# Kernel optimization log

Hardware: AMD Instinct MI355X
Metric: run time of the kernel (lower is better)

The kernel has to match this reference:

```python
import jax, jax.numpy as jnp
import numpy as np

B, S, T, N, D, L = 8192, 10, 3, 65536, 128, 2  # batch, neigh len, node types, table size, embed_d, layers
NEG_SLOPE = 0.01  # torch LeakyReLU default


def setup_inputs() -> dict:
    key = jax.random.key(0)
    ks = jax.random.split(key, 6)
    return {
        "emb": jax.random.normal(ks[0], (T, N, D), jnp.float32) * 0.02,
        "Wih": jax.random.normal(ks[1], (L, T, D, D), jnp.float32) / np.sqrt(D).astype(np.float32),
        "Whh": jax.random.normal(ks[2], (L, T, D, D), jnp.float32) / np.sqrt(D).astype(np.float32),
        "bih": jnp.full((L, T, D), 0.1, jnp.float32),
        "bhh": jnp.full((L, T, D), 0.1, jnp.float32),
        "w_att": jax.random.normal(ks[3], (L, 2 * D), jnp.float32) / np.sqrt(2 * D).astype(np.float32),
        "ids": jax.random.randint(ks[4], (B,), 0, N),
        "neigh_idx": jax.random.randint(ks[5], (T, B, S), 0, N),
    }


def _rnn_mean(x, Wih_l, Whh_l, bih_l, bhh_l):
    """x: [T,B,S,D] neighbor embeds. torch nn.RNN(tanh): h_s = tanh(x_s@Wih^T + bih + h@Whh^T + bhh).
    Returns mean of all hidden states over time: [T,B,D]."""
    xs = jnp.moveaxis(x, 2, 0)  # [S, T, B, D]
    h0 = jnp.zeros((T, B, D), x.dtype)

    def step(h, x_s):
        h = jnp.tanh(jnp.einsum('tbd,ted->tbe', x_s, Wih_l) + bih_l[:, None, :]
                     + jnp.einsum('tbd,ted->tbe', h, Whh_l) + bhh_l[:, None, :])
        return h, h

    _, hs = jax.lax.scan(step, h0, xs)  # [S, T, B, D]
    return hs.mean(axis=0)


def reference(emb, Wih, Whh, bih, bhh, w_att, ids, neigh_idx):
    cur = emb[0][ids]  # [B, D] target node type = 0
    # per-type neighbor gather from base embedding tables (same each layer, as in source)
    neigh = jax.vmap(lambda e, i: e[i])(emb, neigh_idx)  # [T, B, S, D]
    for l in range(L):
        agg = _rnn_mean(neigh, Wih[l], Whh[l], bih[l], bhh[l])  # [T, B, D]
        cands = jnp.moveaxis(jnp.concatenate([cur[None], agg], axis=0), 0, 1)  # [B, 1+T, D]
        feat = jnp.concatenate(
            [jnp.broadcast_to(cur[:, None, :], cands.shape), cands], axis=-1)  # [B, 1+T, 2D]
        scores = feat @ w_att[l]  # [B, 1+T]
        w = jax.nn.softmax(scores, axis=1)[..., None]
        cur = jax.nn.leaky_relu(jnp.sum(w * cands, axis=1), NEG_SLOPE)
    return cur
```

## Files before the change

### kernel.cpp

```cpp
#include <hip/hip_runtime.h>
#include <hip/hip_bf16.h>

#define NB   8192
#define NS   10
#define NT   3
#define NN   65536
#define ND   128
#define NL   2
#define ROWS 32

typedef __attribute__((ext_vector_type(8))) short bf16x8;
typedef __attribute__((ext_vector_type(4))) float f32x4;

__device__ __forceinline__ unsigned int pk2(float lo, float hi) {
    unsigned int r;
    asm("v_cvt_pk_bf16_f32 %0, %1, %2" : "=v"(r) : "v"(lo), "v"(hi));
    return r;
}
__device__ __forceinline__ float tanh_f(float x) {
    float e, r;
    asm("v_exp_f32 %0, %1" : "=v"(e) : "v"(x * 2.88539004f));
    asm("v_rcp_f32 %0, %1" : "=v"(r) : "v"(e + 1.0f));
    return fmaf(-2.0f, r, 1.0f);
}
__device__ __forceinline__ void bar_lgkm() {
    asm volatile("s_waitcnt lgkmcnt(0)\n\ts_barrier" ::: "memory");
}

__global__ __launch_bounds__(512)
void rnn_kernel(const float* __restrict__ emb, const float* __restrict__ Wih,
                const float* __restrict__ Whh, const float* __restrict__ bih,
                const float* __restrict__ bhh, const int* __restrict__ nidx,
                float* __restrict__ agg)
{
    __shared__ __align__(16) char lds[6 * 8192];

    const int bid = blockIdx.x;
    const int t   = bid / (NB / ROWS);
    const int b0  = (bid % (NB / ROWS)) * ROWS;

    const int tid  = threadIdx.x;
    const int wv   = tid >> 6;
    const int lay  = wv >> 2;
    const int lane = tid & 63;
    const int l16  = lane & 15;
    const int lg   = lane >> 4;
    const int e0   = (wv & 3) * 32;
    const int rx   = l16 & 7;

    char* xb = lds;
    char* hb = lds + 16384 + lay * 16384;

    const int srow  = tid >> 4;
    const int sq    = tid & 15;
    const int xaddr = srow * 256 + ((sq ^ (srow & 7)) << 4);

    const int* ip = nidx + ((size_t)t * NB + b0 + srow) * NS;
    int idx_nxt = ip[1];

    float4 P0, P1;
    {
        const float* src = emb + ((size_t)t * NN + ip[0]) * ND + sq * 8;
        P0 = *(const float4*)(src);
        P1 = *(const float4*)(src + 4);
    }

    const float* Wih_lt = Wih + (size_t)(lay * NT + t) * ND * ND;
    const float* Whh_lt = Whh + (size_t)(lay * NT + t) * ND * ND;
    const float* bih_lt = bih + (size_t)(lay * NT + t) * ND;
    const float* bhh_lt = bhh + (size_t)(lay * NT + t) * ND;

    bf16x8 Af[2][8];
    #pragma unroll
    for (int mt = 0; mt < 2; ++mt) {
        #pragma unroll
        for (int kc = 0; kc < 8; ++kc) {
            const float* Wsrc = (kc < 4) ? Wih_lt : Whh_lt;
            const float* srcp = Wsrc + (size_t)(e0 + mt * 16 + l16) * ND + (kc & 3) * 32 + lg * 8;
            float4 p0 = *(const float4*)(srcp);
            float4 p1 = *(const float4*)(srcp + 4);
            int4 a;
            a.x = (int)pk2(p0.x, p0.y);
            a.y = (int)pk2(p0.z, p0.w);
            a.z = (int)pk2(p1.x, p1.y);
            a.w = (int)pk2(p1.z, p1.w);
            Af[mt][kc] = *(bf16x8*)&a;
        }
    }

    f32x4 biasv[2];
    #pragma unroll
    for (int mt = 0; mt < 2; ++mt) {
        int e = e0 + mt * 16 + lg * 4;
        float4 bi = *(const float4*)(bih_lt + e);
        float4 bh = *(const float4*)(bhh_lt + e);
        biasv[mt][0] = bi.x + bh.x;
        biasv[mt][1] = bi.y + bh.y;
        biasv[mt][2] = bi.z + bh.z;
        biasv[mt][3] = bi.w + bh.w;
    }

    const int rowb = l16 * 256;
    int rdch[4];
    #pragma unroll
    for (int c = 0; c < 4; ++c)
        rdch[c] = ((c * 4 + lg) ^ rx) << 4;
    int hwch[2];
    #pragma unroll
    for (int mt = 0; mt < 2; ++mt)
        hwch[mt] = (((((e0 >> 3) + 2 * mt) + (lg >> 1)) ^ rx) << 4) + (lg & 1) * 8;

    f32x4 zero4; zero4[0] = 0.f; zero4[1] = 0.f; zero4[2] = 0.f; zero4[3] = 0.f;
    f32x4 Ag[2][2];
    #pragma unroll
    for (int nt = 0; nt < 2; ++nt) { Ag[nt][0] = zero4; Ag[nt][1] = zero4; }

    #pragma unroll
    for (int s = 0; s < NS; ++s) {
        const int par = (s & 1) * 8192;
        const int ppar = ((s + 1) & 1) * 8192;
        {
            int4 pk;
            pk.x = (int)pk2(P0.x, P0.y);
            pk.y = (int)pk2(P0.z, P0.w);
            pk.z = (int)pk2(P1.x, P1.y);
            pk.w = (int)pk2(P1.z, P1.w);
            *(int4*)(xb + xaddr + par) = pk;
        }
        if (s + 1 < NS) {
            const float* src = emb + ((size_t)t * NN + idx_nxt) * ND + sq * 8;
            P0 = *(const float4*)(src);
            P1 = *(const float4*)(src + 4);
            if (s + 2 < NS) idx_nxt = ip[s + 2];
        }
        bar_lgkm();

        f32x4 acc[2][2];
        #pragma unroll
        for (int nt = 0; nt < 2; ++nt) { acc[nt][0] = biasv[0]; acc[nt][1] = biasv[1]; }

        #pragma unroll
        for (int nt = 0; nt < 2; ++nt)
            #pragma unroll
            for (int c = 0; c < 4; ++c) {
                bf16x8 bf = *(const bf16x8*)(xb + rowb + rdch[c] + nt * 4096 + par);
                acc[nt][0] = __builtin_amdgcn_mfma_f32_16x16x32_bf16(Af[0][c], bf, acc[nt][0], 0, 0, 0);
                acc[nt][1] = __builtin_amdgcn_mfma_f32_16x16x32_bf16(Af[1][c], bf, acc[nt][1], 0, 0, 0);
            }
        if (s > 0) {
            #pragma unroll
            for (int nt = 0; nt < 2; ++nt)
                #pragma unroll
                for (int c = 0; c < 4; ++c) {
                    bf16x8 bf = *(const bf16x8*)(hb + rowb + rdch[c] + nt * 4096 + ppar);
                    acc[nt][0] = __builtin_amdgcn_mfma_f32_16x16x32_bf16(Af[0][c + 4], bf, acc[nt][0], 0, 0, 0);
                    acc[nt][1] = __builtin_amdgcn_mfma_f32_16x16x32_bf16(Af[1][c + 4], bf, acc[nt][1], 0, 0, 0);
                }
        }

        #pragma unroll
        for (int nt = 0; nt < 2; ++nt)
            #pragma unroll
            for (int mt = 0; mt < 2; ++mt) {
                f32x4 h;
                #pragma unroll
                for (int i = 0; i < 4; ++i)
                    h[i] = tanh_f(acc[nt][mt][i]);
                Ag[nt][mt] += h;
                int2 pk;
                pk.x = (int)pk2(h[0], h[1]);
                pk.y = (int)pk2(h[2], h[3]);
                *(int2*)(hb + rowb + hwch[mt] + nt * 4096 + par) = pk;
            }
    }

    float* aggp = agg + ((size_t)(lay * NT + t) * NB + b0) * ND;
    #pragma unroll
    for (int nt = 0; nt < 2; ++nt)
        #pragma unroll
        for (int mt = 0; mt < 2; ++mt) {
            f32x4 v = Ag[nt][mt] * 0.1f;
            *(f32x4*)(aggp + (size_t)(nt * 16 + l16) * ND + e0 + mt * 16 + lg * 4) = v;
        }
}

__global__ __launch_bounds__(256)
void att_kernel(const float* __restrict__ emb, const int* __restrict__ ids,
                const float* __restrict__ w_att, const float* __restrict__ agg,
                float* __restrict__ cur, const int l)
{
    const int wid  = threadIdx.x >> 6;
    const int lane = threadIdx.x & 63;
    const int b    = blockIdx.x * 4 + wid;

    const float* waH  = w_att + l * 2 * ND;
    const float* waT  = waH + ND;
    const float* crow = (l == 0) ? (emb + (size_t)ids[b] * ND) : (cur + (size_t)b * ND);
    const float* ab   = agg + ((size_t)(l * NT) * NB + b) * ND;

    const float c1 = crow[lane], c2 = crow[lane + 64];
    const float h1 = waH[lane],  h2 = waH[lane + 64];
    const float t1 = waT[lane],  t2 = waT[lane + 64];
    float g1[3], g2[3];
    #pragma unroll
    for (int tt = 0; tt < 3; ++tt) {
        g1[tt] = ab[(size_t)tt * NB * ND + lane];
        g2[tt] = ab[(size_t)tt * NB * ND + lane + 64];
    }

    float dH = c1 * h1 + c2 * h2;
    float dc = c1 * t1 + c2 * t2;
    float d0 = g1[0] * t1 + g2[0] * t2;
    float d1 = g1[1] * t1 + g2[1] * t2;
    float d2 = g1[2] * t1 + g2[2] * t2;
    #pragma unroll
    for (int off = 32; off > 0; off >>= 1) {
        dH += __shfl_xor(dH, off);
        dc += __shfl_xor(dc, off);
        d0 += __shfl_xor(d0, off);
        d1 += __shfl_xor(d1, off);
        d2 += __shfl_xor(d2, off);
    }

    float s0 = dH + dc, s1 = dH + d0, s2 = dH + d1, s3 = dH + d2;
    float m  = fmaxf(fmaxf(s0, s1), fmaxf(s2, s3));
    float q0 = __expf(s0 - m), q1 = __expf(s1 - m), q2 = __expf(s2 - m), q3 = __expf(s3 - m);
    float inv = __fdividef(1.0f, q0 + q1 + q2 + q3);
    float w0 = q0 * inv, w1 = q1 * inv, w2 = q2 * inv, w3 = q3 * inv;

    float o1 = w0 * c1 + w1 * g1[0] + w2 * g1[1] + w3 * g1[2];
    float o2 = w0 * c2 + w1 * g2[0] + w2 * g2[1] + w3 * g2[2];
    o1 = (o1 > 0.f) ? o1 : 0.01f * o1;
    o2 = (o2 > 0.f) ? o2 : 0.01f * o2;

    float* orow = cur + (size_t)b * ND;
    orow[lane]      = o1;
    orow[lane + 64] = o2;
}

extern "C" void kernel_launch(void* const* d_in, const int* in_sizes, int n_in,
                              void* d_out, int out_size, void* d_ws, size_t ws_size,
                              hipStream_t stream)
{
    const float* emb  = (const float*)d_in[0];
    const float* Wih  = (const float*)d_in[1];
    const float* Whh  = (const float*)d_in[2];
    const float* bih  = (const float*)d_in[3];
    const float* bhh  = (const float*)d_in[4];
    const float* watt = (const float*)d_in[5];
    const int*   ids  = (const int*)d_in[6];
    const int*   nidx = (const int*)d_in[7];

    float* cur = (float*)d_out;
    float* agg = (float*)d_ws;

    rnn_kernel<<<dim3(NT * (NB / ROWS)), dim3(512), 0, stream>>>(emb, Wih, Whh, bih, bhh, nidx, agg);
    att_kernel<<<dim3(NB / 4), dim3(256), 0, stream>>>(emb, ids, watt, agg, cur, 0);
    att_kernel<<<dim3(NB / 4), dim3(256), 0, stream>>>(emb, ids, watt, agg, cur, 1);
}
```

Measured before the change: 78.77 us.

## Split RNN layers into separate blocks with 2-wave blocks covering 64 outputs each

The RNN kernel now launches one block per (layer, type, row tile), each with 128 threads, instead of one 512-thread block that ran both layers together. Each wave now computes 64 output features, so it holds four weight fragments per k-chunk and reuses each loaded B fragment across four MFMAs. Each thread loads a quarter of an embedding row. This lowers LDS per block and allows more blocks in flight, but each block now gathers the same neighbor embeddings separately for each layer and holds more weight registers per thread.

New measurement: 96.28 us. 22.2% more time.

```diff
diff --git a/kernel.cpp b/kernel.cpp
--- a/kernel.cpp
+++ b/kernel.cpp
@@ -27,52 +27,55 @@
     asm volatile("s_waitcnt lgkmcnt(0)\n\ts_barrier" ::: "memory");
 }
 
-__global__ __launch_bounds__(512)
+__global__ __launch_bounds__(128)
 void rnn_kernel(const float* __restrict__ emb, const float* __restrict__ Wih,
                 const float* __restrict__ Whh, const float* __restrict__ bih,
                 const float* __restrict__ bhh, const int* __restrict__ nidx,
                 float* __restrict__ agg)
 {
-    __shared__ __align__(16) char lds[6 * 8192];
+    __shared__ __align__(16) char lds[4 * 8192];
 
     const int bid = blockIdx.x;
-    const int t   = bid / (NB / ROWS);
+    const int l   = bid / (NT * (NB / ROWS));
+    const int t   = (bid / (NB / ROWS)) % NT;
     const int b0  = (bid % (NB / ROWS)) * ROWS;
 
     const int tid  = threadIdx.x;
     const int wv   = tid >> 6;
-    const int lay  = wv >> 2;
     const int lane = tid & 63;
     const int l16  = lane & 15;
     const int lg   = lane >> 4;
-    const int e0   = (wv & 3) * 32;
+    const int e0   = wv * 64;
     const int rx   = l16 & 7;
 
     char* xb = lds;
-    char* hb = lds + 16384 + lay * 16384;
-
-    const int srow  = tid >> 4;
-    const int sq    = tid & 15;
-    const int xaddr = srow * 256 + ((sq ^ (srow & 7)) << 4);
+    char* hb = lds + 16384;
+
+    const int srow = tid >> 2;
+    const int sq   = tid & 3;
+    const int ssw  = srow & 7;
 
     const int* ip = nidx + ((size_t)t * NB + b0 + srow) * NS;
     int idx_nxt = ip[1];
 
-    float4 P0, P1;
+    float4 P[8];
     {
-        const float* src = emb + ((size_t)t * NN + ip[0]) * ND + sq * 8;
-        P0 = *(const float4*)(src);
-        P1 = *(const float4*)(src + 4);
-    }
-
-    const float* Wih_lt = Wih + (size_t)(lay * NT + t) * ND * ND;
-    const float* Whh_lt = Whh + (size_t)(lay * NT + t) * ND * ND;
-    const float* bih_lt = bih + (size_t)(lay * NT + t) * ND;
-    const float* bhh_lt = bhh + (size_t)(lay * NT + t) * ND;
-
-    bf16x8 Af[2][8];
-    #pragma unroll
-    for (int mt = 0; mt < 2; ++mt) {
+        const float* src = emb + ((size_t)t * NN + ip[0]) * ND + sq * 32;
+        #pragma unroll
+        for (int c = 0; c < 4; ++c) {
+            P[2 * c]     = *(const float4*)(src + c * 8);
+            P[2 * c + 1] = *(const float4*)(src + c * 8 + 4);
+        }
+    }
+
+    const float* Wih_lt = Wih + (size_t)(l * NT + t) * ND * ND;
+    const float* Whh_lt = Whh + (size_t)(l * NT + t) * ND * ND;
+    const float* bih_lt = bih + (size_t)(l * NT + t) * ND;
+    const float* bhh_lt = bhh + (size_t)(l * NT + t) * ND;
+
+    bf16x8 Af[4][8];
+    #pragma unroll
+    for (int mt = 0; mt < 4; ++mt) {
         #pragma unroll
         for (int kc = 0; kc < 8; ++kc) {
             const float* Wsrc = (kc < 4) ? Wih_lt : Whh_lt;
@@ -88,9 +91,9 @@
         }
     }
 
-    f32x4 biasv[2];
-    #pragma unroll
-    for (int mt = 0; mt < 2; ++mt) {
+    f32x4 biasv[4];
+    #pragma unroll
+    for (int mt = 0; mt < 4; ++mt) {
         int e = e0 + mt * 16 + lg * 4;
         float4 bi = *(const float4*)(bih_lt + e);
         float4 bh = *(const float4*)(bhh_lt + e);
@@ -100,68 +103,71 @@
         biasv[mt][3] = bi.w + bh.w;
     }
 
-    const int rowb = l16 * 256;
-    int rdch[4];
-    #pragma unroll
-    for (int c = 0; c < 4; ++c)
-        rdch[c] = ((c * 4 + lg) ^ rx) << 4;
-    int hwch[2];
-    #pragma unroll
-    for (int mt = 0; mt < 2; ++mt)
-        hwch[mt] = (((((e0 >> 3) + 2 * mt) + (lg >> 1)) ^ rx) << 4) + (lg & 1) * 8;
-
     f32x4 zero4; zero4[0] = 0.f; zero4[1] = 0.f; zero4[2] = 0.f; zero4[3] = 0.f;
-    f32x4 Ag[2][2];
-    #pragma unroll
-    for (int nt = 0; nt < 2; ++nt) { Ag[nt][0] = zero4; Ag[nt][1] = zero4; }
+    f32x4 Ag[2][4];
+    #pragma unroll
+    for (int nt = 0; nt < 2; ++nt)
+        #pragma unroll
+        for (int mt = 0; mt < 4; ++mt) Ag[nt][mt] = zero4;
 
     #pragma unroll
     for (int s = 0; s < NS; ++s) {
-        const int par = (s & 1) * 8192;
+        const int par  = (s & 1) * 8192;
         const int ppar = ((s + 1) & 1) * 8192;
-        {
+
+        #pragma unroll
+        for (int c = 0; c < 4; ++c) {
             int4 pk;
-            pk.x = (int)pk2(P0.x, P0.y);
-            pk.y = (int)pk2(P0.z, P0.w);
-            pk.z = (int)pk2(P1.x, P1.y);
-            pk.w = (int)pk2(P1.z, P1.w);
-            *(int4*)(xb + xaddr + par) = pk;
+            pk.x = (int)pk2(P[2 * c].x,     P[2 * c].y);
+            pk.y = (int)pk2(P[2 * c].z,     P[2 * c].w);
+            pk.z = (int)pk2(P[2 * c + 1].x, P[2 * c + 1].y);
+            pk.w = (int)pk2(P[2 * c + 1].z, P[2 * c + 1].w);
+            *(int4*)(xb + srow * 256 + (((sq * 4 + c) ^ ssw) << 4) + par) = pk;
         }
         if (s + 1 < NS) {
-            const float* src = emb + ((size_t)t * NN + idx_nxt) * ND + sq * 8;
-            P0 = *(const float4*)(src);
-            P1 = *(const float4*)(src + 4);
+            const float* src = emb + ((size_t)t * NN + idx_nxt) * ND + sq * 32;
+            #pragma unroll
+            for (int c = 0; c < 4; ++c) {
+                P[2 * c]     = *(const float4*)(src + c * 8);
+                P[2 * c + 1] = *(const float4*)(src + c * 8 + 4);
+            }
             if (s + 2 < NS) idx_nxt = ip[s + 2];
         }
         bar_lgkm();
 
-        f32x4 acc[2][2];
-        #pragma unroll
-        for (int nt = 0; nt < 2; ++nt) { acc[nt][0] = biasv[0]; acc[nt][1] = biasv[1]; }
-
+        f32x4 acc[2][4];
         #pragma unroll
         for (int nt = 0; nt < 2; ++nt)
             #pragma unroll
+            for (int mt = 0; mt < 4; ++mt) acc[nt][mt] = biasv[mt];
+
+        #pragma unroll
+        for (int nt = 0; nt < 2; ++nt)
+            #pragma unroll
             for (int c = 0; c < 4; ++c) {
-                bf16x8 bf = *(const bf16x8*)(xb + rowb + rdch[c] + nt * 4096 + par);
-                acc[nt][0] = __builtin_amdgcn_mfma_f32_16x16x32_bf16(Af[0][c], bf, acc[nt][0], 0, 0, 0);
-                acc[nt][1] = __builtin_amdgcn_mfma_f32_16x16x32_bf16(Af[1][c], bf, acc[nt][1], 0, 0, 0);
+                bf16x8 bf = *(const bf16x8*)(xb + nt * 4096 + l16 * 256
+                                             + (((c * 4 + lg) ^ rx) << 4) + par);
+                #pragma unroll
+                for (int mt = 0; mt < 4; ++mt)
+                    acc[nt][mt] = __builtin_amdgcn_mfma_f32_16x16x32_bf16(Af[mt][c], bf, acc[nt][mt], 0, 0, 0);
             }
         if (s > 0) {
             #pragma unroll
             for (int nt = 0; nt < 2; ++nt)
                 #pragma unroll
                 for (int c = 0; c < 4; ++c) {
-                    bf16x8 bf = *(const bf16x8*)(hb + rowb + rdch[c] + nt * 4096 + ppar);
-                    acc[nt][0] = __builtin_amdgcn_mfma_f32_16x16x32_bf16(Af[0][c + 4], bf, acc[nt][0], 0, 0, 0);
-                    acc[nt][1] = __builtin_amdgcn_mfma_f32_16x16x32_bf16(Af[1][c + 4], bf, acc[nt][1], 0, 0, 0);
+                    bf16x8 bf = *(const bf16x8*)(hb + nt * 4096 + l16 * 256
+                                                 + (((c * 4 + lg) ^ rx) << 4) + ppar);
+                    #pragma unroll
+                    for (int mt = 0; mt < 4; ++mt)
+                        acc[nt][mt] = __builtin_amdgcn_mfma_f32_16x16x32_bf16(Af[mt][c + 4], bf, acc[nt][mt], 0, 0, 0);
                 }
         }
 
         #pragma unroll
         for (int nt = 0; nt < 2; ++nt)
             #pragma unroll
-            for (int mt = 0; mt < 2; ++mt) {
+            for (int mt = 0; mt < 4; ++mt) {
                 f32x4 h;
                 #pragma unroll
                 for (int i = 0; i < 4; ++i)
@@ -170,15 +176,17 @@
                 int2 pk;
                 pk.x = (int)pk2(h[0], h[1]);
                 pk.y = (int)pk2(h[2], h[3]);
-                *(int2*)(hb + rowb + hwch[mt] + nt * 4096 + par) = pk;
+                int es = e0 + mt * 16 + lg * 4;
+                *(int2*)(hb + nt * 4096 + l16 * 256
+                         + ((((es >> 3)) ^ rx) << 4) + (lg & 1) * 8 + par) = pk;
             }
     }
 
-    float* aggp = agg + ((size_t)(lay * NT + t) * NB + b0) * ND;
+    float* aggp = agg + ((size_t)(l * NT + t) * NB + b0) * ND;
     #pragma unroll
     for (int nt = 0; nt < 2; ++nt)
         #pragma unroll
-        for (int mt = 0; mt < 2; ++mt) {
+        for (int mt = 0; mt < 4; ++mt) {
             f32x4 v = Ag[nt][mt] * 0.1f;
             *(f32x4*)(aggp + (size_t)(nt * 16 + l16) * ND + e0 + mt * 16 + lg * 4) = v;
         }
@@ -254,7 +262,7 @@
     float* cur = (float*)d_out;
     float* agg = (float*)d_ws;
 
-    rnn_kernel<<<dim3(NT * (NB / ROWS)), dim3(512), 0, stream>>>(emb, Wih, Whh, bih, bhh, nidx, agg);
+    rnn_kernel<<<dim3(NL * NT * (NB / ROWS)), dim3(128), 0, stream>>>(emb, Wih, Whh, bih, bhh, nidx, agg);
     att_kernel<<<dim3(NB / 4), dim3(256), 0, stream>>>(emb, ids, watt, agg, cur, 0);
     att_kernel<<<dim3(NB / 4), dim3(256), 0, stream>>>(emb, ids, watt, agg, cur, 1);
 }
```
